# Optimization experiments

Hardware: AMD Instinct MI355X
Metric: run time of the kernel (lower is better)

The kernel has to match this reference:

```python
import jax, jax.numpy as jnp
import numpy as np

INPUT_DIM = 1024
HIDDEN_DIM = 1024
CHUNK_SIZE = 4


def _linear_params(key, fan_in, fan_out):
    kw, kb = jax.random.split(key)
    bound = 1.0 / np.sqrt(fan_in)
    W = jax.random.uniform(kw, (fan_in, fan_out), jnp.float32, -bound, bound)
    b = jax.random.uniform(kb, (fan_out,), jnp.float32, -bound, bound)
    return W, b


def setup_inputs() -> dict:
    key = jax.random.key(0)
    ks = jax.random.split(key, 6)
    x = jax.random.normal(ks[0], (64, 512, INPUT_DIM), jnp.float32)
    h0 = jax.random.normal(ks[1], (64, HIDDEN_DIM), jnp.float32)
    Wz, bz = _linear_params(ks[2], INPUT_DIM + HIDDEN_DIM, HIDDEN_DIM)
    Wr, br = _linear_params(ks[3], INPUT_DIM + HIDDEN_DIM, HIDDEN_DIM)
    Wh, bh = _linear_params(ks[4], INPUT_DIM + HIDDEN_DIM, HIDDEN_DIM)
    Wp, bp = _linear_params(ks[5], HIDDEN_DIM, HIDDEN_DIM)
    return {"x": x, "h0": h0, "Wz": Wz, "bz": bz, "Wr": Wr, "br": br,
            "Wh": Wh, "bh": bh, "Wp": Wp, "bp": bp}


def _gru_forward(x, h0, Wz, bz, Wr, br, Wh, bh, Wp, bp):
    B, T, D = x.shape
    # seq_len chosen divisible by CHUNK_SIZE, so no padding needed.
    t = jnp.arange(T)
    # propagate state through tanh(Linear) at chunk boundaries, except after last chunk
    do_prop = (((t + 1) % CHUNK_SIZE) == 0) & (t < T - 1)  # [T] bool

    xs = jnp.transpose(x, (1, 0, 2))  # [T, B, D]

    def step(h, inp):
        x_t, prop = inp  # x_t: [B, D], prop: scalar bool
        comb = jnp.concatenate([x_t, h], axis=-1)          # [B, D+H]
        z = jax.nn.sigmoid(comb @ Wz + bz)
        r = jax.nn.sigmoid(comb @ Wr + br)
        comb2 = jnp.concatenate([x_t, r * h], axis=-1)
        h_cand = jnp.tanh(comb2 @ Wh + bh)
        h_new = (1.0 - z) * h + z * h_cand                 # output for this step
        h_next = jnp.where(prop, jnp.tanh(h_new @ Wp + bp), h_new)
        return h_next, h_new

    _, ys = jax.lax.scan(step, h0, (xs, do_prop))          # ys: [T, B, H]
    return jnp.transpose(ys, (1, 0, 2))                    # [B, T, H]


def reference(x, h0, Wz, bz, Wr, br, Wh, bh, Wp, bp):
    return _gru_forward(x, h0, Wz, bz, Wr, br, Wh, bh, Wp, bp)
```

## Files before the change

kernel.cpp:

```cpp
#include <hip/hip_runtime.h>
#include <hip/hip_fp16.h>


typedef _Float16 half8 __attribute__((ext_vector_type(8)));
typedef _Float16 half4v __attribute__((ext_vector_type(4)));
typedef float    floatx4 __attribute__((ext_vector_type(4)));

#define T_STEPS 512

#define AL(p)    __hip_atomic_load((p), __ATOMIC_RELAXED, __HIP_MEMORY_SCOPE_AGENT)
#define AS(p, v) __hip_atomic_store((p), (v), __ATOMIC_RELAXED, __HIP_MEMORY_SCOPE_AGENT)
#define AADD(p)  __hip_atomic_fetch_add((p), 1u, __ATOMIC_RELAXED, __HIP_MEMORY_SCOPE_AGENT)

union U16 { unsigned long long u[2]; half8 h; };

__device__ __forceinline__ void poll_cnt(const unsigned* c, unsigned target) {
    unsigned v = AL(c);
    while (v < target) {
        if (target - v > 8u) __builtin_amdgcn_s_sleep(2);
        v = AL(c);
    }
    asm volatile("" ::: "memory");
}

__global__ void pack_wxT(const float* __restrict__ Wz, const float* __restrict__ Wr,
                         const float* __restrict__ Wh, _Float16* __restrict__ wxT) {
    __shared__ float tile[64][65];
    const int k0 = blockIdx.x * 64;
    const int c0 = blockIdx.y * 64;
    const int gate = blockIdx.z;
    const float* W = (gate == 0) ? Wz : ((gate == 1) ? Wr : Wh);
    const int tid = threadIdx.x;
    const int tc = tid & 63;
    const int tr = tid >> 6;
#pragma unroll
    for (int rr = 0; rr < 16; ++rr) {
        int kr = rr * 4 + tr;
        tile[kr][tc] = W[(size_t)(k0 + kr) * 1024 + c0 + tc];
    }
    __syncthreads();
#pragma unroll
    for (int rr = 0; rr < 16; ++rr) {
        int nr = rr * 4 + tr;
        wxT[(size_t)(gate * 1024 + c0 + nr) * 1024 + k0 + tc] = (_Float16)tile[tc][nr];
    }
}

__global__ void pack_wrec(const float* __restrict__ Wz, const float* __restrict__ Wr,
                          const float* __restrict__ Wh, const float* __restrict__ Wp,
                          _Float16* __restrict__ wpack) {
    int idx = blockIdx.x * 256 + threadIdx.x;
    int mat = (idx >> 11) & 3;
    int kk = (idx >> 6) & 31;
    int lane = idx & 63;
    int j = idx >> 13;
    int n = j * 16 + (lane & 15);
    int kb = kk * 32 + (lane >> 4) * 8;
    const float* W = (mat == 0) ? Wz : ((mat == 1) ? Wr : ((mat == 2) ? Wh : Wp));
    size_t rowoff = (mat < 3) ? 1024 : 0;
#pragma unroll
    for (int e = 0; e < 8; ++e)
        wpack[(size_t)idx * 8 + e] = (_Float16)W[(rowoff + kb + e) * 1024 + n];
}

__global__ void init_misc(const float* __restrict__ h0, _Float16* __restrict__ hfrag,
                          unsigned* __restrict__ flags) {
    int idx = blockIdx.x * 256 + threadIdx.x;
    int g = idx >> 11;
    int kk = (idx >> 6) & 31;
    int lane = idx & 63;
    int b = lane & 15;
    int kb = kk * 32 + (lane >> 4) * 8;
#pragma unroll
    for (int e = 0; e < 8; ++e)
        hfrag[(size_t)g * 16384 + (size_t)(kk * 64 + lane) * 8 + e] =
            (_Float16)h0[(size_t)(g * 16 + b) * 1024 + kb + e];
    if (blockIdx.x == 0) {
        flags[threadIdx.x] = 0;
        flags[threadIdx.x + 256] = 0;
        flags[threadIdx.x + 512] = 0;
    }
}

__global__ __launch_bounds__(256) void xproj_gemm(
    const float* __restrict__ x, const _Float16* __restrict__ wxT,
    const float* __restrict__ bz, const float* __restrict__ br,
    const float* __restrict__ bh, _Float16* __restrict__ Xtmp) {
    __shared__ _Float16 Als[128][40];
    __shared__ _Float16 Bls[128][40];
    const int tid = threadIdx.x;
    const int n0 = blockIdx.x * 128;
    const int m0 = blockIdx.y * 128;
    const int lane = tid & 63;
    const int wave = tid >> 6;
    const int lm = lane & 15, lq = lane >> 4;
    const int wm = (wave >> 1) * 64, wn = (wave & 1) * 64;
    const int srow = tid >> 1;
    const int shalf = (tid & 1) * 16;

    floatx4 acc[4][4];
#pragma unroll
    for (int mi = 0; mi < 4; ++mi)
#pragma unroll
        for (int ni = 0; ni < 4; ++ni) acc[mi][ni] = (floatx4){0.f, 0.f, 0.f, 0.f};

    for (int k0 = 0; k0 < 1024; k0 += 32) {
        {
            const float* src = x + (size_t)(m0 + srow) * 1024 + k0 + shalf;
            float4 p0 = ((const float4*)src)[0];
            float4 p1 = ((const float4*)src)[1];
            float4 p2 = ((const float4*)src)[2];
            float4 p3 = ((const float4*)src)[3];
            half8 h0v = {(_Float16)p0.x, (_Float16)p0.y, (_Float16)p0.z, (_Float16)p0.w,
                         (_Float16)p1.x, (_Float16)p1.y, (_Float16)p1.z, (_Float16)p1.w};
            half8 h1v = {(_Float16)p2.x, (_Float16)p2.y, (_Float16)p2.z, (_Float16)p2.w,
                         (_Float16)p3.x, (_Float16)p3.y, (_Float16)p3.z, (_Float16)p3.w};
            *(half8*)&Als[srow][shalf] = h0v;
            *(half8*)&Als[srow][shalf + 8] = h1v;
            const _Float16* bsrc = wxT + (size_t)(n0 + srow) * 1024 + k0 + shalf;
            *(half8*)&Bls[srow][shalf] = ((const half8*)bsrc)[0];
            *(half8*)&Bls[srow][shalf + 8] = ((const half8*)bsrc)[1];
        }
        __syncthreads();
        half8 af[4], bf[4];
#pragma unroll
        for (int mi = 0; mi < 4; ++mi) af[mi] = *(const half8*)&Als[wm + mi * 16 + lm][lq * 8];
#pragma unroll
        for (int ni = 0; ni < 4; ++ni) bf[ni] = *(const half8*)&Bls[wn + ni * 16 + lm][lq * 8];
#pragma unroll
        for (int mi = 0; mi < 4; ++mi)
#pragma unroll
            for (int ni = 0; ni < 4; ++ni)
                acc[mi][ni] = __builtin_amdgcn_mfma_f32_16x16x32_f16(af[mi], bf[ni], acc[mi][ni], 0, 0, 0);
        __syncthreads();
    }
#pragma unroll
    for (int mi = 0; mi < 4; ++mi) {
#pragma unroll
        for (int i = 0; i < 4; ++i) {
            int row = m0 + wm + mi * 16 + lq * 4 + i;
            int t = row & 511;
            int bglob = row >> 9;
            int g = bglob >> 4, b = bglob & 15;
#pragma unroll
            for (int ni = 0; ni < 4; ++ni) {
                int col = n0 + wn + ni * 16 + lm;
                int mat = col >> 10;
                int jc = col - mat * 1024;
                int jj = jc >> 4, c = jc & 15;
                float bias = (mat == 0) ? bz[jc] : ((mat == 1) ? br[jc] : bh[jc]);
                size_t idx = ((((size_t)(g * 64 + jj) * 3 + mat) * 512 + t) << 8) + c * 16 + b;
                Xtmp[idx] = (_Float16)(acc[mi][ni][i] + bias);
            }
        }
    }
}

__global__ __launch_bounds__(256, 1) void gru_seq_kernel(
    const _Float16* __restrict__ Xtmp, const _Float16* __restrict__ wpack,
    const float* __restrict__ h0,
    _Float16* __restrict__ hfrag,
    _Float16* __restrict__ rfrag,
    _Float16* __restrict__ hnfrag,
    unsigned* flags_h, unsigned* flags_r, unsigned* flags_n,
    const float* __restrict__ bp, float* __restrict__ out) {
    const int wg = blockIdx.x;
    const int g = wg & 3;
    const int j = wg >> 2;
    const int tid = threadIdx.x;
    const int wave = tid >> 6;
    const int lane = tid & 63;
    const int lm = lane & 15;
    const int lq = lane >> 4;

    __shared__ __align__(16) _Float16 als[32 * 64 * 8];
    __shared__ float zbuf[256];
    __shared__ float pbuf[256];
    __shared__ _Float16 rbuf[256];
    __shared__ _Float16 hbuf[256];
    __shared__ _Float16 nbuf[256];

    half8 W[32];
    {
        const half8* wp = (const half8*)wpack + (size_t)((j * 4 + wave) * 32) * 64 + lane;
#pragma unroll
        for (int kk = 0; kk < 32; ++kk) W[kk] = wp[kk * 64];
    }
    const float bpl = bp[j * 16 + lm];

    unsigned* ch = flags_h + g * 64;
    unsigned* cr = flags_r + g * 64;
    unsigned* cn = flags_n + g * 64;

    const int kkd = j >> 1;
    const int s_ = lane >> 5;
    const int b_ = (lane >> 1) & 15;
    const int hp_ = lane & 1;
    const size_t fidx = (size_t)((kkd * 64 + (2 * (j & 1) + s_) * 16 + b_) * 2 + hp_);
    const int ldsrd = b_ * 16 + s_ * 8 + hp_ * 4;

    float hreg[4];
    if (wave == 2) {
#pragma unroll
        for (int i = 0; i < 4; ++i)
            hreg[i] = h0[(size_t)(g * 16 + lq * 4 + i) * 1024 + j * 16 + lm];
    }

    unsigned long long* als8 = (unsigned long long*)als;

    for (int t = 0; t < T_STEPS; ++t) {
        const bool boundary = ((t & 3) == 3) && (t != T_STEPS - 1);

        if (wave < 2) {
            poll_cnt(ch, 64u * (unsigned)t);
            const unsigned long long* hp8 =
                (const unsigned long long*)(hfrag + (size_t)((t & 1) * 4 + g) * 16384);
            unsigned long long tmp[32];
            const int base = wave * 16;
#pragma unroll
            for (int q = 0; q < 16; ++q) {
                int kk = base + q;
                tmp[2 * q] = AL(hp8 + (size_t)(kk * 64 + lane) * 2);
                tmp[2 * q + 1] = AL(hp8 + (size_t)(kk * 64 + lane) * 2 + 1);
            }
#pragma unroll
            for (int q = 0; q < 16; ++q) {
                int kk = base + q;
                als8[(kk * 64 + lane) * 2] = tmp[2 * q];
                als8[(kk * 64 + lane) * 2 + 1] = tmp[2 * q + 1];
            }
        }
        __syncthreads();

        if (wave < 2) {
            half4v xv4 = *(const half4v*)(Xtmp +
                ((((size_t)(g * 64 + j) * 3 + wave) * 512 + t) << 8) + lm * 16 + lq * 4);
            floatx4 acc = {0.f, 0.f, 0.f, 0.f};
#pragma unroll
            for (int kk = 0; kk < 32; ++kk) {
                half8 av = *(const half8*)&als[(kk * 64 + lane) * 8];
                acc = __builtin_amdgcn_mfma_f32_16x16x32_f16(av, W[kk], acc, 0, 0, 0);
            }
            if (wave == 0) {
#pragma unroll
                for (int i = 0; i < 4; ++i)
                    zbuf[lane * 4 + i] = 1.f / (1.f + __expf(-(acc[i] + (float)xv4[i])));
            } else {
#pragma unroll
                for (int i = 0; i < 4; ++i)
                    rbuf[(lq * 4 + i) * 16 + lm] =
                        (_Float16)(1.f / (1.f + __expf(-(acc[i] + (float)xv4[i]))));
                asm volatile("s_waitcnt lgkmcnt(0)" ::: "memory");
                unsigned long long rv8 = *(const unsigned long long*)&rbuf[ldsrd];
                AS((unsigned long long*)(rfrag + (size_t)g * 16384) + fidx, rv8);
                asm volatile("s_waitcnt vmcnt(0)" ::: "memory");
                if (lane == 0) AADD(cr);
            }
        }
        __syncthreads();

        if (wave == 2) {
            half4v xv4 = *(const half4v*)(Xtmp +
                ((((size_t)(g * 64 + j) * 3 + 2) * 512 + t) << 8) + lm * 16 + lq * 4);
            poll_cnt(cr, 64u * (unsigned)(t + 1));
            const unsigned long long* rr8 = (const unsigned long long*)(rfrag + (size_t)g * 16384);
            unsigned long long rtmp[64];
#pragma unroll
            for (int kk = 0; kk < 32; ++kk) {
                rtmp[2 * kk]     = AL(rr8 + (size_t)(kk * 64 + lane) * 2);
                rtmp[2 * kk + 1] = AL(rr8 + (size_t)(kk * 64 + lane) * 2 + 1);
            }
            floatx4 acc = {0.f, 0.f, 0.f, 0.f};
#pragma unroll
            for (int kk = 0; kk < 32; ++kk) {
                half8 av = *(const half8*)&als[(kk * 64 + lane) * 8];
                U16 rc;
                rc.u[0] = rtmp[2 * kk];
                rc.u[1] = rtmp[2 * kk + 1];
                half8 prod = av * rc.h;
                acc = __builtin_amdgcn_mfma_f32_16x16x32_f16(prod, W[kk], acc, 0, 0, 0);
            }
            const bool post_b = (t > 0) && ((t & 3) == 0);
            float hn_[4];
#pragma unroll
            for (int i = 0; i < 4; ++i) {
                float hp = post_b ? pbuf[(lq * 4 + i) * 16 + lm] : hreg[i];
                float z = zbuf[lane * 4 + i];
                float hc = tanhf(acc[i] + (float)xv4[i]);
                float hn = (1.f - z) * hp + z * hc;
                hn_[i] = hn;
                hreg[i] = hn;
                hbuf[(lq * 4 + i) * 16 + lm] = (_Float16)hn;
            }
            asm volatile("s_waitcnt lgkmcnt(0)" ::: "memory");
            unsigned long long hv8 = *(const unsigned long long*)&hbuf[ldsrd];
            unsigned long long* dst8 = (unsigned long long*)(boundary
                ? (hnfrag + (size_t)g * 16384)
                : (hfrag + (size_t)(((t + 1) & 1) * 4 + g) * 16384));
            AS(dst8 + fidx, hv8);
            asm volatile("s_waitcnt vmcnt(0)" ::: "memory");
            if (t < T_STEPS - 1 && lane == 0) {
                if (boundary) AADD(cn);
                else          AADD(ch);
            }
#pragma unroll
            for (int i = 0; i < 4; ++i)
                __builtin_nontemporal_store(hn_[i],
                    &out[(size_t)((g * 16 + lq * 4 + i) * 512 + t) * 1024 + j * 16 + lm]);
        } else if (wave == 3 && boundary) {
            poll_cnt(cn, 64u * (unsigned)((t + 1) >> 2));
            const unsigned long long* nn8 = (const unsigned long long*)(hnfrag + (size_t)g * 16384);
            unsigned long long ntmp[64];
#pragma unroll
            for (int kk = 0; kk < 32; ++kk) {
                ntmp[2 * kk]     = AL(nn8 + (size_t)(kk * 64 + lane) * 2);
                ntmp[2 * kk + 1] = AL(nn8 + (size_t)(kk * 64 + lane) * 2 + 1);
            }
            floatx4 acc = {0.f, 0.f, 0.f, 0.f};
#pragma unroll
            for (int kk = 0; kk < 32; ++kk) {
                U16 nc;
                nc.u[0] = ntmp[2 * kk];
                nc.u[1] = ntmp[2 * kk + 1];
                acc = __builtin_amdgcn_mfma_f32_16x16x32_f16(nc.h, W[kk], acc, 0, 0, 0);
            }
#pragma unroll
            for (int i = 0; i < 4; ++i) {
                float hv = tanhf(acc[i] + bpl);
                pbuf[(lq * 4 + i) * 16 + lm] = hv;
                nbuf[(lq * 4 + i) * 16 + lm] = (_Float16)hv;
            }
            asm volatile("s_waitcnt lgkmcnt(0)" ::: "memory");
            unsigned long long nv8 = *(const unsigned long long*)&nbuf[ldsrd];
            AS((unsigned long long*)(hfrag + (size_t)(((t + 1) & 1) * 4 + g) * 16384) + fidx, nv8);
            asm volatile("s_waitcnt vmcnt(0)" ::: "memory");
            if (lane == 0) AADD(ch);
        }
    }
}

extern "C" void kernel_launch(void* const* d_in, const int* in_sizes, int n_in,
                              void* d_out, int out_size, void* d_ws, size_t ws_size,
                              hipStream_t stream) {
    (void)in_sizes; (void)n_in; (void)out_size; (void)ws_size;
    const float* x  = (const float*)d_in[0];
    const float* h0 = (const float*)d_in[1];
    const float* Wz = (const float*)d_in[2];
    const float* bz = (const float*)d_in[3];
    const float* Wr = (const float*)d_in[4];
    const float* br = (const float*)d_in[5];
    const float* Wh = (const float*)d_in[6];
    const float* bh = (const float*)d_in[7];
    const float* Wp = (const float*)d_in[8];
    const float* bp = (const float*)d_in[9];
    float* out = (float*)d_out;

    char* ws = (char*)d_ws;
    _Float16* wxT    = (_Float16*)(ws);
    _Float16* wpack  = (_Float16*)(ws + 6291456);
    _Float16* Xtmp   = (_Float16*)(ws + 14680064);
    _Float16* hfrag  = (_Float16*)(ws + 216006656);
    _Float16* rfrag  = (_Float16*)(ws + 216268800);
    _Float16* hnfrag = (_Float16*)(ws + 216399872);
    unsigned* flags  = (unsigned*)(ws + 216530944);
    unsigned* flags_h = flags;
    unsigned* flags_r = flags + 256;
    unsigned* flags_n = flags + 512;

    pack_wxT<<<dim3(16, 16, 3), 256, 0, stream>>>(Wz, Wr, Wh, wxT);
    pack_wrec<<<2048, 256, 0, stream>>>(Wz, Wr, Wh, Wp, wpack);
    init_misc<<<32, 256, 0, stream>>>(h0, hfrag, flags);
    xproj_gemm<<<dim3(24, 256), 256, 0, stream>>>(x, wxT, bz, br, bh, Xtmp);
    gru_seq_kernel<<<256, 256, 0, stream>>>(Xtmp, wpack, h0, hfrag, rfrag, hnfrag,
                                            flags_h, flags_r, flags_n, bp, out);
}
```

Before: 6.436 ms.

## Merge four column-slice workgroups into one block with shared h/r staging

The recurrent kernel now launches 64 blocks of 1024 threads. Each block handles four hidden-column slices, so the h and r fragments are loaded from global memory once per block into LDS and shared by all four slices, instead of once per slice. Global flag increments are aggregated in LDS so only the fourth arriving wave bumps the global counter by four, and a single thread polls the global counter and then releases the others through a workgroup-scope token. MFMA chains are split into two independent accumulators to shorten dependency latency. The trade-off is more __syncthreads per step across 16 waves and fewer, larger blocks on the device.

```diff
diff --git a/kernel.cpp b/kernel.cpp
--- a/kernel.cpp
+++ b/kernel.cpp
@@ -8,9 +8,9 @@
 
 #define T_STEPS 512
 
-#define AL(p)    __hip_atomic_load((p), __ATOMIC_RELAXED, __HIP_MEMORY_SCOPE_AGENT)
-#define AS(p, v) __hip_atomic_store((p), (v), __ATOMIC_RELAXED, __HIP_MEMORY_SCOPE_AGENT)
-#define AADD(p)  __hip_atomic_fetch_add((p), 1u, __ATOMIC_RELAXED, __HIP_MEMORY_SCOPE_AGENT)
+#define AL(p)     __hip_atomic_load((p), __ATOMIC_RELAXED, __HIP_MEMORY_SCOPE_AGENT)
+#define AS(p, v)  __hip_atomic_store((p), (v), __ATOMIC_RELAXED, __HIP_MEMORY_SCOPE_AGENT)
+#define AADD4(p)  __hip_atomic_fetch_add((p), 4u, __ATOMIC_RELAXED, __HIP_MEMORY_SCOPE_AGENT)
 
 union U16 { unsigned long long u[2]; half8 h; };
 
@@ -20,6 +20,12 @@
         if (target - v > 8u) __builtin_amdgcn_s_sleep(2);
         v = AL(c);
     }
+    asm volatile("" ::: "memory");
+}
+
+__device__ __forceinline__ void spin_tok(unsigned* tok, unsigned target) {
+    while (__hip_atomic_load(tok, __ATOMIC_RELAXED, __HIP_MEMORY_SCOPE_WORKGROUP) < target)
+        __builtin_amdgcn_s_sleep(1);
     asm volatile("" ::: "memory");
 }
 
@@ -156,7 +162,7 @@
     }
 }
 
-__global__ __launch_bounds__(256, 1) void gru_seq_kernel(
+__global__ __launch_bounds__(1024, 1) void gru_seq_kernel(
     const _Float16* __restrict__ Xtmp, const _Float16* __restrict__ wpack,
     const float* __restrict__ h0,
     _Float16* __restrict__ hfrag,
@@ -164,25 +170,32 @@
     _Float16* __restrict__ hnfrag,
     unsigned* flags_h, unsigned* flags_r, unsigned* flags_n,
     const float* __restrict__ bp, float* __restrict__ out) {
-    const int wg = blockIdx.x;
-    const int g = wg & 3;
-    const int j = wg >> 2;
+    const int g = blockIdx.x & 3;
+    const int J = blockIdx.x >> 2;
     const int tid = threadIdx.x;
-    const int wave = tid >> 6;
+    const int w = tid >> 6;
     const int lane = tid & 63;
+    const int role = w >> 2;
+    const int s = w & 3;
+    const int j = J * 4 + s;
     const int lm = lane & 15;
     const int lq = lane >> 4;
 
     __shared__ __align__(16) _Float16 als[32 * 64 * 8];
-    __shared__ float zbuf[256];
-    __shared__ float pbuf[256];
-    __shared__ _Float16 rbuf[256];
-    __shared__ _Float16 hbuf[256];
-    __shared__ _Float16 nbuf[256];
+    __shared__ __align__(16) _Float16 rls[32 * 64 * 8];
+    __shared__ float zbuf[4][256];
+    __shared__ float pbuf[4][256];
+    __shared__ _Float16 rbuf[4][256];
+    __shared__ _Float16 hbuf[4][256];
+    __shared__ _Float16 nbuf[4][256];
+    __shared__ unsigned tokR, tokN, lds_ch, lds_cr, lds_cn;
+
+    if (tid == 0) { tokR = 0u; tokN = 0u; lds_ch = 0u; lds_cr = 0u; lds_cn = 0u; }
+    __syncthreads();
 
     half8 W[32];
     {
-        const half8* wp = (const half8*)wpack + (size_t)((j * 4 + wave) * 32) * 64 + lane;
+        const half8* wp = (const half8*)wpack + (size_t)((j * 4 + role) * 32) * 64 + lane;
 #pragma unroll
         for (int kk = 0; kk < 32; ++kk) W[kk] = wp[kk * 64];
     }
@@ -200,141 +213,179 @@
     const int ldsrd = b_ * 16 + s_ * 8 + hp_ * 4;
 
     float hreg[4];
-    if (wave == 2) {
+    if (role == 2) {
 #pragma unroll
         for (int i = 0; i < 4; ++i)
             hreg[i] = h0[(size_t)(g * 16 + lq * 4 + i) * 1024 + j * 16 + lm];
     }
 
     unsigned long long* als8 = (unsigned long long*)als;
+    unsigned long long* rls8 = (unsigned long long*)rls;
 
     for (int t = 0; t < T_STEPS; ++t) {
         const bool boundary = ((t & 3) == 3) && (t != T_STEPS - 1);
 
-        if (wave < 2) {
-            poll_cnt(ch, 64u * (unsigned)t);
+        if (tid == 0) poll_cnt(ch, 64u * (unsigned)t);
+        __syncthreads();
+
+        {
             const unsigned long long* hp8 =
                 (const unsigned long long*)(hfrag + (size_t)((t & 1) * 4 + g) * 16384);
-            unsigned long long tmp[32];
-            const int base = wave * 16;
-#pragma unroll
-            for (int q = 0; q < 16; ++q) {
-                int kk = base + q;
-                tmp[2 * q] = AL(hp8 + (size_t)(kk * 64 + lane) * 2);
-                tmp[2 * q + 1] = AL(hp8 + (size_t)(kk * 64 + lane) * 2 + 1);
-            }
-#pragma unroll
-            for (int q = 0; q < 16; ++q) {
-                int kk = base + q;
-                als8[(kk * 64 + lane) * 2] = tmp[2 * q];
-                als8[(kk * 64 + lane) * 2 + 1] = tmp[2 * q + 1];
-            }
-        }
-        __syncthreads();
-
-        if (wave < 2) {
+            const int kk0 = w * 2, kk1 = w * 2 + 1;
+            unsigned long long a0 = AL(hp8 + (size_t)(kk0 * 64 + lane) * 2);
+            unsigned long long a1 = AL(hp8 + (size_t)(kk0 * 64 + lane) * 2 + 1);
+            unsigned long long b0 = AL(hp8 + (size_t)(kk1 * 64 + lane) * 2);
+            unsigned long long b1 = AL(hp8 + (size_t)(kk1 * 64 + lane) * 2 + 1);
+            als8[(kk0 * 64 + lane) * 2] = a0;
+            als8[(kk0 * 64 + lane) * 2 + 1] = a1;
+            als8[(kk1 * 64 + lane) * 2] = b0;
+            als8[(kk1 * 64 + lane) * 2 + 1] = b1;
+        }
+        __syncthreads();
+
+        if (role < 2) {
             half4v xv4 = *(const half4v*)(Xtmp +
-                ((((size_t)(g * 64 + j) * 3 + wave) * 512 + t) << 8) + lm * 16 + lq * 4);
-            floatx4 acc = {0.f, 0.f, 0.f, 0.f};
-#pragma unroll
-            for (int kk = 0; kk < 32; ++kk) {
-                half8 av = *(const half8*)&als[(kk * 64 + lane) * 8];
-                acc = __builtin_amdgcn_mfma_f32_16x16x32_f16(av, W[kk], acc, 0, 0, 0);
-            }
-            if (wave == 0) {
+                ((((size_t)(g * 64 + j) * 3 + role) * 512 + t) << 8) + lm * 16 + lq * 4);
+            floatx4 a0 = {0.f, 0.f, 0.f, 0.f}, a1 = {0.f, 0.f, 0.f, 0.f};
+#pragma unroll
+            for (int kk = 0; kk < 32; kk += 2) {
+                half8 av0 = *(const half8*)&als[(kk * 64 + lane) * 8];
+                half8 av1 = *(const half8*)&als[((kk + 1) * 64 + lane) * 8];
+                a0 = __builtin_amdgcn_mfma_f32_16x16x32_f16(av0, W[kk], a0, 0, 0, 0);
+                a1 = __builtin_amdgcn_mfma_f32_16x16x32_f16(av1, W[kk + 1], a1, 0, 0, 0);
+            }
+            floatx4 acc = a0 + a1;
+            if (role == 0) {
 #pragma unroll
                 for (int i = 0; i < 4; ++i)
-                    zbuf[lane * 4 + i] = 1.f / (1.f + __expf(-(acc[i] + (float)xv4[i])));
+                    zbuf[s][lane * 4 + i] = 1.f / (1.f + __expf(-(acc[i] + (float)xv4[i])));
             } else {
 #pragma unroll
                 for (int i = 0; i < 4; ++i)
-                    rbuf[(lq * 4 + i) * 16 + lm] =
+                    rbuf[s][(lq * 4 + i) * 16 + lm] =
                         (_Float16)(1.f / (1.f + __expf(-(acc[i] + (float)xv4[i]))));
                 asm volatile("s_waitcnt lgkmcnt(0)" ::: "memory");
-                unsigned long long rv8 = *(const unsigned long long*)&rbuf[ldsrd];
+                unsigned long long rv8 = *(const unsigned long long*)&rbuf[s][ldsrd];
                 AS((unsigned long long*)(rfrag + (size_t)g * 16384) + fidx, rv8);
                 asm volatile("s_waitcnt vmcnt(0)" ::: "memory");
-                if (lane == 0) AADD(cr);
-            }
-        }
-        __syncthreads();
-
-        if (wave == 2) {
+                if (lane == 0) {
+                    unsigned old = atomicAdd(&lds_cr, 1u);
+                    if ((old & 3u) == 3u) AADD4(cr);
+                }
+            }
+        }
+        __syncthreads();
+
+        if (role == 2) {
+            if (s == 0 && lane == 0) {
+                poll_cnt(cr, 64u * (unsigned)(t + 1));
+                __hip_atomic_store(&tokR, (unsigned)(t + 1), __ATOMIC_RELAXED,
+                                   __HIP_MEMORY_SCOPE_WORKGROUP);
+            }
+            spin_tok(&tokR, (unsigned)(t + 1));
+            const unsigned long long* rr8 =
+                (const unsigned long long*)(rfrag + (size_t)g * 16384);
+            unsigned long long tmp[16];
+#pragma unroll
+            for (int q = 0; q < 8; ++q) {
+                int kk = s * 8 + q;
+                tmp[2 * q]     = AL(rr8 + (size_t)(kk * 64 + lane) * 2);
+                tmp[2 * q + 1] = AL(rr8 + (size_t)(kk * 64 + lane) * 2 + 1);
+            }
+#pragma unroll
+            for (int q = 0; q < 8; ++q) {
+                int kk = s * 8 + q;
+                rls8[(kk * 64 + lane) * 2] = tmp[2 * q];
+                rls8[(kk * 64 + lane) * 2 + 1] = tmp[2 * q + 1];
+            }
+        }
+        __syncthreads();
+
+        if (role == 2) {
             half4v xv4 = *(const half4v*)(Xtmp +
                 ((((size_t)(g * 64 + j) * 3 + 2) * 512 + t) << 8) + lm * 16 + lq * 4);
-            poll_cnt(cr, 64u * (unsigned)(t + 1));
-            const unsigned long long* rr8 = (const unsigned long long*)(rfrag + (size_t)g * 16384);
-            unsigned long long rtmp[64];
-#pragma unroll
-            for (int kk = 0; kk < 32; ++kk) {
-                rtmp[2 * kk]     = AL(rr8 + (size_t)(kk * 64 + lane) * 2);
-                rtmp[2 * kk + 1] = AL(rr8 + (size_t)(kk * 64 + lane) * 2 + 1);
-            }
-            floatx4 acc = {0.f, 0.f, 0.f, 0.f};
-#pragma unroll
-            for (int kk = 0; kk < 32; ++kk) {
-                half8 av = *(const half8*)&als[(kk * 64 + lane) * 8];
-                U16 rc;
-                rc.u[0] = rtmp[2 * kk];
-                rc.u[1] = rtmp[2 * kk + 1];
-                half8 prod = av * rc.h;
-                acc = __builtin_amdgcn_mfma_f32_16x16x32_f16(prod, W[kk], acc, 0, 0, 0);
-            }
+            floatx4 a0 = {0.f, 0.f, 0.f, 0.f}, a1 = {0.f, 0.f, 0.f, 0.f};
+#pragma unroll
+            for (int kk = 0; kk < 32; kk += 2) {
+                half8 av0 = *(const half8*)&als[(kk * 64 + lane) * 8];
+                half8 rc0 = *(const half8*)&rls[(kk * 64 + lane) * 8];
+                half8 av1 = *(const half8*)&als[((kk + 1) * 64 + lane) * 8];
+                half8 rc1 = *(const half8*)&rls[((kk + 1) * 64 + lane) * 8];
+                a0 = __builtin_amdgcn_mfma_f32_16x16x32_f16(av0 * rc0, W[kk], a0, 0, 0, 0);
+                a1 = __builtin_amdgcn_mfma_f32_16x16x32_f16(av1 * rc1, W[kk + 1], a1, 0, 0, 0);
+            }
+            floatx4 acc = a0 + a1;
             const bool post_b = (t > 0) && ((t & 3) == 0);
             float hn_[4];
 #pragma unroll
             for (int i = 0; i < 4; ++i) {
-                float hp = post_b ? pbuf[(lq * 4 + i) * 16 + lm] : hreg[i];
-                float z = zbuf[lane * 4 + i];
+                float hp = post_b ? pbuf[s][(lq * 4 + i) * 16 + lm] : hreg[i];
+                float z = zbuf[s][lane * 4 + i];
                 float hc = tanhf(acc[i] + (float)xv4[i]);
                 float hn = (1.f - z) * hp + z * hc;
                 hn_[i] = hn;
                 hreg[i] = hn;
-                hbuf[(lq * 4 + i) * 16 + lm] = (_Float16)hn;
+                hbuf[s][(lq * 4 + i) * 16 + lm] = (_Float16)hn;
             }
             asm volatile("s_waitcnt lgkmcnt(0)" ::: "memory");
-            unsigned long long hv8 = *(const unsigned long long*)&hbuf[ldsrd];
+            unsigned long long hv8 = *(const unsigned long long*)&hbuf[s][ldsrd];
             unsigned long long* dst8 = (unsigned long long*)(boundary
                 ? (hnfrag + (size_t)g * 16384)
                 : (hfrag + (size_t)(((t + 1) & 1) * 4 + g) * 16384));
             AS(dst8 + fidx, hv8);
             asm volatile("s_waitcnt vmcnt(0)" ::: "memory");
             if (t < T_STEPS - 1 && lane == 0) {
-                if (boundary) AADD(cn);
-                else          AADD(ch);
+                if (boundary) {
+                    unsigned old = atomicAdd(&lds_cn, 1u);
+                    if ((old & 3u) == 3u) AADD4(cn);
+                } else {
+                    unsigned old = atomicAdd(&lds_ch, 1u);
+                    if ((old & 3u) == 3u) AADD4(ch);
+                }
             }
 #pragma unroll
             for (int i = 0; i < 4; ++i)
                 __builtin_nontemporal_store(hn_[i],
                     &out[(size_t)((g * 16 + lq * 4 + i) * 512 + t) * 1024 + j * 16 + lm]);
-        } else if (wave == 3 && boundary) {
-            poll_cnt(cn, 64u * (unsigned)((t + 1) >> 2));
-            const unsigned long long* nn8 = (const unsigned long long*)(hnfrag + (size_t)g * 16384);
+        } else if (role == 3 && boundary) {
+            if (s == 0 && lane == 0) {
+                poll_cnt(cn, 64u * (unsigned)((t + 1) >> 2));
+                __hip_atomic_store(&tokN, (unsigned)((t + 1) >> 2), __ATOMIC_RELAXED,
+                                   __HIP_MEMORY_SCOPE_WORKGROUP);
+            }
+            spin_tok(&tokN, (unsigned)((t + 1) >> 2));
+            const unsigned long long* nn8 =
+                (const unsigned long long*)(hnfrag + (size_t)g * 16384);
             unsigned long long ntmp[64];
 #pragma unroll
             for (int kk = 0; kk < 32; ++kk) {
                 ntmp[2 * kk]     = AL(nn8 + (size_t)(kk * 64 + lane) * 2);
                 ntmp[2 * kk + 1] = AL(nn8 + (size_t)(kk * 64 + lane) * 2 + 1);
             }
-            floatx4 acc = {0.f, 0.f, 0.f, 0.f};
-#pragma unroll
-            for (int kk = 0; kk < 32; ++kk) {
-                U16 nc;
-                nc.u[0] = ntmp[2 * kk];
-                nc.u[1] = ntmp[2 * kk + 1];
-                acc = __builtin_amdgcn_mfma_f32_16x16x32_f16(nc.h, W[kk], acc, 0, 0, 0);
-            }
+            floatx4 a0 = {0.f, 0.f, 0.f, 0.f}, a1 = {0.f, 0.f, 0.f, 0.f};
+#pragma unroll
+            for (int kk = 0; kk < 32; kk += 2) {
+                U16 nc0, nc1;
+                nc0.u[0] = ntmp[2 * kk];     nc0.u[1] = ntmp[2 * kk + 1];
+                nc1.u[0] = ntmp[2 * kk + 2]; nc1.u[1] = ntmp[2 * kk + 3];
+                a0 = __builtin_amdgcn_mfma_f32_16x16x32_f16(nc0.h, W[kk], a0, 0, 0, 0);
+                a1 = __builtin_amdgcn_mfma_f32_16x16x32_f16(nc1.h, W[kk + 1], a1, 0, 0, 0);
+            }
+            floatx4 acc = a0 + a1;
 #pragma unroll
             for (int i = 0; i < 4; ++i) {
                 float hv = tanhf(acc[i] + bpl);
-                pbuf[(lq * 4 + i) * 16 + lm] = hv;
-                nbuf[(lq * 4 + i) * 16 + lm] = (_Float16)hv;
+                pbuf[s][(lq * 4 + i) * 16 + lm] = hv;
+                nbuf[s][(lq * 4 + i) * 16 + lm] = (_Float16)hv;
             }
             asm volatile("s_waitcnt lgkmcnt(0)" ::: "memory");
-            unsigned long long nv8 = *(const unsigned long long*)&nbuf[ldsrd];
+            unsigned long long nv8 = *(const unsigned long long*)&nbuf[s][ldsrd];
             AS((unsigned long long*)(hfrag + (size_t)(((t + 1) & 1) * 4 + g) * 16384) + fidx, nv8);
             asm volatile("s_waitcnt vmcnt(0)" ::: "memory");
-            if (lane == 0) AADD(ch);
+            if (lane == 0) {
+                unsigned old = atomicAdd(&lds_ch, 1u);
+                if ((old & 3u) == 3u) AADD4(ch);
+            }
         }
     }
 }
@@ -371,6 +422,6 @@
     pack_wrec<<<2048, 256, 0, stream>>>(Wz, Wr, Wh, Wp, wpack);
     init_misc<<<32, 256, 0, stream>>>(h0, hfrag, flags);
     xproj_gemm<<<dim3(24, 256), 256, 0, stream>>>(x, wxT, bz, br, bh, Xtmp);
-    gru_seq_kernel<<<256, 256, 0, stream>>>(Xtmp, wpack, h0, hfrag, rfrag, hnfrag,
+    gru_seq_kernel<<<64, 1024, 0, stream>>>(Xtmp, wpack, h0, hfrag, rfrag, hnfrag,
                                             flags_h, flags_r, flags_n, bp, out);
 }
```

Result: slower. 11.96 ms (+85.8%).

## Split step counters four ways, stage hidden state with all waves, dual MFMA accumulators

Applied to the files above, without the earlier changes.

Each group's single arrival counter becomes four sub-counters spaced 16 words apart. Producers increment one of them based on j, and consumers poll all four with a wave-wide __all check, which reduces atomic contention on one cache line. Staging of the h fragment into LDS now uses all four waves after a single poll by wave 0, where two waves did it before. The MFMA reductions use two independent accumulators to shorten the dependency chain. In exchange there are extra __syncthreads per step and more polling traffic.

```diff
diff --git a/kernel.cpp b/kernel.cpp
--- a/kernel.cpp
+++ b/kernel.cpp
@@ -10,18 +10,36 @@
 
 #define AL(p)    __hip_atomic_load((p), __ATOMIC_RELAXED, __HIP_MEMORY_SCOPE_AGENT)
 #define AS(p, v) __hip_atomic_store((p), (v), __ATOMIC_RELAXED, __HIP_MEMORY_SCOPE_AGENT)
-#define AADD(p)  __hip_atomic_fetch_add((p), 1u, __ATOMIC_RELAXED, __HIP_MEMORY_SCOPE_AGENT)
+#define AADD1(p) __hip_atomic_fetch_add((p), 1u, __ATOMIC_RELAXED, __HIP_MEMORY_SCOPE_AGENT)
 
 union U16 { unsigned long long u[2]; half8 h; };
 
-__device__ __forceinline__ void poll_cnt(const unsigned* c, unsigned target) {
-    unsigned v = AL(c);
-    while (v < target) {
-        if (target - v > 8u) __builtin_amdgcn_s_sleep(2);
-        v = AL(c);
+__device__ __forceinline__ void poll4(const unsigned* base, unsigned target, int lane) {
+    const unsigned* p = base + (lane & 3) * 16;
+    while (true) {
+        unsigned v = AL(p);
+        if (__all(v >= target)) break;
+        __builtin_amdgcn_s_sleep(1);
     }
     asm volatile("" ::: "memory");
 }
+
+#define STAGE8(SRCP, DSTP)                                                 \
+    {                                                                      \
+        const unsigned long long* s8 = (const unsigned long long*)(SRCP);  \
+        unsigned long long* d8 = (unsigned long long*)(DSTP);              \
+        unsigned long long tmp[16];                                        \
+        _Pragma("unroll") for (int q = 0; q < 8; ++q) {                    \
+            int kk = wave * 8 + q;                                         \
+            tmp[2 * q]     = AL(s8 + (size_t)(kk * 64 + lane) * 2);        \
+            tmp[2 * q + 1] = AL(s8 + (size_t)(kk * 64 + lane) * 2 + 1);    \
+        }                                                                  \
+        _Pragma("unroll") for (int q = 0; q < 8; ++q) {                    \
+            int kk = wave * 8 + q;                                         \
+            d8[(kk * 64 + lane) * 2]     = tmp[2 * q];                     \
+            d8[(kk * 64 + lane) * 2 + 1] = tmp[2 * q + 1];                 \
+        }                                                                  \
+    }
 
 __global__ void pack_wxT(const float* __restrict__ Wz, const float* __restrict__ Wr,
                          const float* __restrict__ Wh, _Float16* __restrict__ wxT) {
@@ -191,6 +209,7 @@
     unsigned* ch = flags_h + g * 64;
     unsigned* cr = flags_r + g * 64;
     unsigned* cn = flags_n + g * 64;
+    const int sub = (j & 3) * 16;
 
     const int kkd = j >> 1;
     const int s_ = lane >> 5;
@@ -206,41 +225,27 @@
             hreg[i] = h0[(size_t)(g * 16 + lq * 4 + i) * 1024 + j * 16 + lm];
     }
 
-    unsigned long long* als8 = (unsigned long long*)als;
-
     for (int t = 0; t < T_STEPS; ++t) {
         const bool boundary = ((t & 3) == 3) && (t != T_STEPS - 1);
 
-        if (wave < 2) {
-            poll_cnt(ch, 64u * (unsigned)t);
-            const unsigned long long* hp8 =
-                (const unsigned long long*)(hfrag + (size_t)((t & 1) * 4 + g) * 16384);
-            unsigned long long tmp[32];
-            const int base = wave * 16;
-#pragma unroll
-            for (int q = 0; q < 16; ++q) {
-                int kk = base + q;
-                tmp[2 * q] = AL(hp8 + (size_t)(kk * 64 + lane) * 2);
-                tmp[2 * q + 1] = AL(hp8 + (size_t)(kk * 64 + lane) * 2 + 1);
-            }
-#pragma unroll
-            for (int q = 0; q < 16; ++q) {
-                int kk = base + q;
-                als8[(kk * 64 + lane) * 2] = tmp[2 * q];
-                als8[(kk * 64 + lane) * 2 + 1] = tmp[2 * q + 1];
-            }
-        }
+        if (wave == 0) poll4(ch, 16u * (unsigned)t, lane);
+        __syncthreads();
+
+        STAGE8(hfrag + (size_t)((t & 1) * 4 + g) * 16384, als);
         __syncthreads();
 
         if (wave < 2) {
             half4v xv4 = *(const half4v*)(Xtmp +
                 ((((size_t)(g * 64 + j) * 3 + wave) * 512 + t) << 8) + lm * 16 + lq * 4);
-            floatx4 acc = {0.f, 0.f, 0.f, 0.f};
-#pragma unroll
-            for (int kk = 0; kk < 32; ++kk) {
-                half8 av = *(const half8*)&als[(kk * 64 + lane) * 8];
-                acc = __builtin_amdgcn_mfma_f32_16x16x32_f16(av, W[kk], acc, 0, 0, 0);
-            }
+            floatx4 a0 = {0.f, 0.f, 0.f, 0.f}, a1 = {0.f, 0.f, 0.f, 0.f};
+#pragma unroll
+            for (int kk = 0; kk < 32; kk += 2) {
+                half8 av0 = *(const half8*)&als[(kk * 64 + lane) * 8];
+                half8 av1 = *(const half8*)&als[((kk + 1) * 64 + lane) * 8];
+                a0 = __builtin_amdgcn_mfma_f32_16x16x32_f16(av0, W[kk], a0, 0, 0, 0);
+                a1 = __builtin_amdgcn_mfma_f32_16x16x32_f16(av1, W[kk + 1], a1, 0, 0, 0);
+            }
+            floatx4 acc = a0 + a1;
             if (wave == 0) {
 #pragma unroll
                 for (int i = 0; i < 4; ++i)
@@ -254,7 +259,7 @@
                 unsigned long long rv8 = *(const unsigned long long*)&rbuf[ldsrd];
                 AS((unsigned long long*)(rfrag + (size_t)g * 16384) + fidx, rv8);
                 asm volatile("s_waitcnt vmcnt(0)" ::: "memory");
-                if (lane == 0) AADD(cr);
+                if (lane == 0) AADD1(cr + sub);
             }
         }
         __syncthreads();
@@ -262,7 +267,7 @@
         if (wave == 2) {
             half4v xv4 = *(const half4v*)(Xtmp +
                 ((((size_t)(g * 64 + j) * 3 + 2) * 512 + t) << 8) + lm * 16 + lq * 4);
-            poll_cnt(cr, 64u * (unsigned)(t + 1));
+            poll4(cr, 16u * (unsigned)(t + 1), lane);
             const unsigned long long* rr8 = (const unsigned long long*)(rfrag + (size_t)g * 16384);
             unsigned long long rtmp[64];
 #pragma unroll
@@ -270,16 +275,18 @@
                 rtmp[2 * kk]     = AL(rr8 + (size_t)(kk * 64 + lane) * 2);
                 rtmp[2 * kk + 1] = AL(rr8 + (size_t)(kk * 64 + lane) * 2 + 1);
             }
-            floatx4 acc = {0.f, 0.f, 0.f, 0.f};
-#pragma unroll
-            for (int kk = 0; kk < 32; ++kk) {
-                half8 av = *(const half8*)&als[(kk * 64 + lane) * 8];
-                U16 rc;
-                rc.u[0] = rtmp[2 * kk];
-                rc.u[1] = rtmp[2 * kk + 1];
-                half8 prod = av * rc.h;
-                acc = __builtin_amdgcn_mfma_f32_16x16x32_f16(prod, W[kk], acc, 0, 0, 0);
-            }
+            floatx4 a0 = {0.f, 0.f, 0.f, 0.f}, a1 = {0.f, 0.f, 0.f, 0.f};
+#pragma unroll
+            for (int kk = 0; kk < 32; kk += 2) {
+                half8 av0 = *(const half8*)&als[(kk * 64 + lane) * 8];
+                half8 av1 = *(const half8*)&als[((kk + 1) * 64 + lane) * 8];
+                U16 rc0, rc1;
+                rc0.u[0] = rtmp[2 * kk];     rc0.u[1] = rtmp[2 * kk + 1];
+                rc1.u[0] = rtmp[2 * kk + 2]; rc1.u[1] = rtmp[2 * kk + 3];
+                a0 = __builtin_amdgcn_mfma_f32_16x16x32_f16(av0 * rc0.h, W[kk], a0, 0, 0, 0);
+                a1 = __builtin_amdgcn_mfma_f32_16x16x32_f16(av1 * rc1.h, W[kk + 1], a1, 0, 0, 0);
+            }
+            floatx4 acc = a0 + a1;
             const bool post_b = (t > 0) && ((t & 3) == 0);
             float hn_[4];
 #pragma unroll
@@ -300,15 +307,15 @@
             AS(dst8 + fidx, hv8);
             asm volatile("s_waitcnt vmcnt(0)" ::: "memory");
             if (t < T_STEPS - 1 && lane == 0) {
-                if (boundary) AADD(cn);
-                else          AADD(ch);
+                if (boundary) AADD1(cn + sub);
+                else          AADD1(ch + sub);
             }
 #pragma unroll
             for (int i = 0; i < 4; ++i)
                 __builtin_nontemporal_store(hn_[i],
                     &out[(size_t)((g * 16 + lq * 4 + i) * 512 + t) * 1024 + j * 16 + lm]);
         } else if (wave == 3 && boundary) {
-            poll_cnt(cn, 64u * (unsigned)((t + 1) >> 2));
+            poll4(cn, 16u * (unsigned)((t + 1) >> 2), lane);
             const unsigned long long* nn8 = (const unsigned long long*)(hnfrag + (size_t)g * 16384);
             unsigned long long ntmp[64];
 #pragma unroll
@@ -316,14 +323,16 @@
                 ntmp[2 * kk]     = AL(nn8 + (size_t)(kk * 64 + lane) * 2);
                 ntmp[2 * kk + 1] = AL(nn8 + (size_t)(kk * 64 + lane) * 2 + 1);
             }
-            floatx4 acc = {0.f, 0.f, 0.f, 0.f};
-#pragma unroll
-            for (int kk = 0; kk < 32; ++kk) {
-                U16 nc;
-                nc.u[0] = ntmp[2 * kk];
-                nc.u[1] = ntmp[2 * kk + 1];
-                acc = __builtin_amdgcn_mfma_f32_16x16x32_f16(nc.h, W[kk], acc, 0, 0, 0);
-            }
+            floatx4 a0 = {0.f, 0.f, 0.f, 0.f}, a1 = {0.f, 0.f, 0.f, 0.f};
+#pragma unroll
+            for (int kk = 0; kk < 32; kk += 2) {
+                U16 nc0, nc1;
+                nc0.u[0] = ntmp[2 * kk];     nc0.u[1] = ntmp[2 * kk + 1];
+                nc1.u[0] = ntmp[2 * kk + 2]; nc1.u[1] = ntmp[2 * kk + 3];
+                a0 = __builtin_amdgcn_mfma_f32_16x16x32_f16(nc0.h, W[kk], a0, 0, 0, 0);
+                a1 = __builtin_amdgcn_mfma_f32_16x16x32_f16(nc1.h, W[kk + 1], a1, 0, 0, 0);
+            }
+            floatx4 acc = a0 + a1;
 #pragma unroll
             for (int i = 0; i < 4; ++i) {
                 float hv = tanhf(acc[i] + bpl);
@@ -334,7 +343,7 @@
             unsigned long long nv8 = *(const unsigned long long*)&nbuf[ldsrd];
             AS((unsigned long long*)(hfrag + (size_t)(((t + 1) & 1) * 4 + g) * 16384) + fidx, nv8);
             asm volatile("s_waitcnt vmcnt(0)" ::: "memory");
-            if (lane == 0) AADD(ch);
+            if (lane == 0) AADD1(ch + sub);
         }
     }
 }
```

New measurement: 7.052 ms. 1.1x slower.

## Replace workgroup barrier with LDS token handshake between the two gate waves

Applied to the files above, without the earlier changes.

Removes the __syncthreads between staging h into LDS and the MFMA loop. Each of the two gate waves instead publishes an LDS token once its half is written and starts multiplying its own half right away. It then spins on the other wave's token before consuming the remaining half. The MFMA chain is also split into two independent accumulators to shorten the dependency chain, and the x load is hoisted above the h load. The risks are correctness issues with relaxed LDS ordering and spin cost, and the other waves no longer synchronize at this point.

```diff
diff --git a/kernel.cpp b/kernel.cpp
--- a/kernel.cpp
+++ b/kernel.cpp
@@ -21,6 +21,13 @@
         v = AL(c);
     }
     asm volatile("" ::: "memory");
+}
+
+__device__ __forceinline__ void spin_tok(const unsigned* tok, unsigned target) {
+    while (__hip_atomic_load(tok, __ATOMIC_RELAXED, __HIP_MEMORY_SCOPE_WORKGROUP) < target)
+        ;
+    asm volatile("" ::: "memory");
+    __builtin_amdgcn_sched_barrier(0);
 }
 
 __global__ void pack_wxT(const float* __restrict__ Wz, const float* __restrict__ Wr,
@@ -179,6 +186,10 @@
     __shared__ _Float16 rbuf[256];
     __shared__ _Float16 hbuf[256];
     __shared__ _Float16 nbuf[256];
+    __shared__ unsigned tok0, tok1;
+
+    if (tid == 0) { tok0 = 0u; tok1 = 0u; }
+    __syncthreads();
 
     half8 W[32];
     {
@@ -213,34 +224,50 @@
 
         if (wave < 2) {
             poll_cnt(ch, 64u * (unsigned)t);
+            half4v xv4 = *(const half4v*)(Xtmp +
+                ((((size_t)(g * 64 + j) * 3 + wave) * 512 + t) << 8) + lm * 16 + lq * 4);
             const unsigned long long* hp8 =
                 (const unsigned long long*)(hfrag + (size_t)((t & 1) * 4 + g) * 16384);
-            unsigned long long tmp[32];
-            const int base = wave * 16;
-#pragma unroll
-            for (int q = 0; q < 16; ++q) {
-                int kk = base + q;
-                tmp[2 * q] = AL(hp8 + (size_t)(kk * 64 + lane) * 2);
-                tmp[2 * q + 1] = AL(hp8 + (size_t)(kk * 64 + lane) * 2 + 1);
-            }
-#pragma unroll
-            for (int q = 0; q < 16; ++q) {
-                int kk = base + q;
-                als8[(kk * 64 + lane) * 2] = tmp[2 * q];
-                als8[(kk * 64 + lane) * 2 + 1] = tmp[2 * q + 1];
-            }
-        }
-        __syncthreads();
-
-        if (wave < 2) {
-            half4v xv4 = *(const half4v*)(Xtmp +
-                ((((size_t)(g * 64 + j) * 3 + wave) * 512 + t) << 8) + lm * 16 + lq * 4);
-            floatx4 acc = {0.f, 0.f, 0.f, 0.f};
-#pragma unroll
-            for (int kk = 0; kk < 32; ++kk) {
-                half8 av = *(const half8*)&als[(kk * 64 + lane) * 8];
-                acc = __builtin_amdgcn_mfma_f32_16x16x32_f16(av, W[kk], acc, 0, 0, 0);
-            }
+            const int ownb = wave * 16;
+            const int othb = 16 - ownb;
+            {
+                unsigned long long tmp[32];
+#pragma unroll
+                for (int q = 0; q < 16; ++q) {
+                    int kk = ownb + q;
+                    tmp[2 * q]     = AL(hp8 + (size_t)(kk * 64 + lane) * 2);
+                    tmp[2 * q + 1] = AL(hp8 + (size_t)(kk * 64 + lane) * 2 + 1);
+                }
+#pragma unroll
+                for (int q = 0; q < 16; ++q) {
+                    int kk = ownb + q;
+                    als8[(kk * 64 + lane) * 2] = tmp[2 * q];
+                    als8[(kk * 64 + lane) * 2 + 1] = tmp[2 * q + 1];
+                }
+            }
+            asm volatile("s_waitcnt lgkmcnt(0)" ::: "memory");
+            if (lane == 0)
+                __hip_atomic_store(wave == 0 ? &tok0 : &tok1, (unsigned)(t + 1),
+                                   __ATOMIC_RELAXED, __HIP_MEMORY_SCOPE_WORKGROUP);
+            floatx4 a0 = {0.f, 0.f, 0.f, 0.f}, a1 = {0.f, 0.f, 0.f, 0.f};
+#pragma unroll
+            for (int q = 0; q < 16; q += 2) {
+                int kk = ownb + q;
+                half8 av0 = *(const half8*)&als[(kk * 64 + lane) * 8];
+                half8 av1 = *(const half8*)&als[((kk + 1) * 64 + lane) * 8];
+                a0 = __builtin_amdgcn_mfma_f32_16x16x32_f16(av0, W[kk], a0, 0, 0, 0);
+                a1 = __builtin_amdgcn_mfma_f32_16x16x32_f16(av1, W[kk + 1], a1, 0, 0, 0);
+            }
+            spin_tok(wave == 0 ? &tok1 : &tok0, (unsigned)(t + 1));
+#pragma unroll
+            for (int q = 0; q < 16; q += 2) {
+                int kk = othb + q;
+                half8 av0 = *(const half8*)&als[(kk * 64 + lane) * 8];
+                half8 av1 = *(const half8*)&als[((kk + 1) * 64 + lane) * 8];
+                a0 = __builtin_amdgcn_mfma_f32_16x16x32_f16(av0, W[kk], a0, 0, 0, 0);
+                a1 = __builtin_amdgcn_mfma_f32_16x16x32_f16(av1, W[kk + 1], a1, 0, 0, 0);
+            }
+            floatx4 acc = a0 + a1;
             if (wave == 0) {
 #pragma unroll
                 for (int i = 0; i < 4; ++i)
```

Measured after the change: 7.993 ms. 24.2% more time.
